# Optimization experiments

Measured on AMD Instinct MI355X. Metric: run time of the kernel, lower is better.

The kernel has to match this reference:

```python
import jax, jax.numpy as jnp
import numpy as np

N, F_IN, HID, H1, E = 50000, 512, 128, 4, 800000
NEG_SLOPE = 0.2

def setup_inputs() -> dict:
    key = jax.random.key(0)
    ks = jax.random.split(key, 10)
    s = lambda fan: 1.0 / np.sqrt(fan)
    x = jax.random.normal(ks[0], (N, F_IN), jnp.float32)
    edge_index = jax.random.randint(ks[1], (2, E), 0, N, jnp.int32)
    W1 = jax.random.normal(ks[2], (F_IN, H1 * HID), jnp.float32) * s(F_IN)
    a_src1 = jax.random.normal(ks[3], (H1, HID), jnp.float32) * s(HID)
    a_dst1 = jax.random.normal(ks[4], (H1, HID), jnp.float32) * s(HID)
    b1 = jnp.zeros((H1 * HID,), jnp.float32)
    W2 = jax.random.normal(ks[5], (H1 * HID, HID), jnp.float32) * s(H1 * HID)
    a_src2 = jax.random.normal(ks[6], (1, HID), jnp.float32) * s(HID)
    a_dst2 = jax.random.normal(ks[7], (1, HID), jnp.float32) * s(HID)
    b2 = jnp.zeros((HID,), jnp.float32)
    return {"x": x, "edge_index": edge_index, "W1": W1, "a_src1": a_src1,
            "a_dst1": a_dst1, "b1": b1, "W2": W2, "a_src2": a_src2,
            "a_dst2": a_dst2, "b2": b2}

def _gat(x, src, dst, W, a_src, a_dst, b, n):
    H, C = a_src.shape
    h = (x @ W).reshape(-1, H, C)                      # [N, H, C]
    # per-edge attention logits: alpha_src[src] + alpha_dst[dst]
    e = jax.nn.leaky_relu((h * a_src).sum(-1)[src] + (h * a_dst).sum(-1)[dst],
                          NEG_SLOPE)                   # [E', H]
    # segment softmax over destination node
    m = jax.ops.segment_max(e, dst, num_segments=n)
    p = jnp.exp(e - m[dst])
    denom = jax.ops.segment_sum(p, dst, num_segments=n)
    alpha = p / (denom[dst] + 1e-16)
    # weighted scatter-add aggregation
    out = jax.ops.segment_sum(h[src] * alpha[:, :, None], dst, num_segments=n)
    return out.reshape(-1, H * C) + b

def reference(x, edge_index, W1, a_src1, a_dst1, b1, W2, a_src2, a_dst2, b2):
    loops = jnp.arange(N, dtype=edge_index.dtype)      # add_self_loops=True
    src = jnp.concatenate([edge_index[0], loops])
    dst = jnp.concatenate([edge_index[1], loops])
    h = jax.nn.elu(_gat(x, src, dst, W1, a_src1, a_dst1, b1, N))
    return _gat(h, src, dst, W2, a_src2, a_dst2, b2, N)
```

## Files before the change

### kernel.cpp

```cpp
#include <hip/hip_runtime.h>
#include <hip/hip_bf16.h>
#include <math.h>

#define NEG_SLOPE 0.2f

constexpr int N_NODES = 50000;
constexpr int F_IN    = 512;
constexpr int HID     = 128;
constexpr int H1      = 4;
constexpr int E_EDGES = 800000;
constexpr int E_TOT   = E_EDGES + N_NODES;
constexpr int DEG_CAP = 64;

typedef __attribute__((ext_vector_type(8))) short short8;
typedef __attribute__((ext_vector_type(4))) float floatx4;
typedef __attribute__((ext_vector_type(2))) float f32x2;
typedef __attribute__((ext_vector_type(4))) unsigned short ushort4v;

__device__ __forceinline__ unsigned short f2bf(float f) {
  union { float f; unsigned int u; } v; v.f = f;
  unsigned int u = v.u + 0x7FFFu + ((v.u >> 16) & 1u);
  return (unsigned short)(u >> 16);
}
__device__ __forceinline__ float bf_lo(unsigned int u) {
  union { unsigned int u; float f; } v; v.u = u << 16; return v.f;
}
__device__ __forceinline__ float bf_hi(unsigned int u) {
  union { unsigned int u; float f; } v; v.u = u & 0xFFFF0000u; return v.f;
}

__device__ __forceinline__ void store_val(float* p, float v) { *p = v; }
__device__ __forceinline__ void store_val(unsigned short* p, float v) { *p = f2bf(v); }

template <int CPT>
__device__ __forceinline__ void store_vec(unsigned short* p, const float* v) {
#pragma unroll
  for (int c = 0; c < CPT; c += 4) {
    ushort4v o;
#pragma unroll
    for (int j = 0; j < 4; ++j) o[j] = f2bf(v[c + j]);
    *(ushort4v*)(p + c) = o;
  }
}
template <int CPT>
__device__ __forceinline__ void store_vec(float* p, const float* v) {
#pragma unroll
  for (int c = 0; c < CPT; c += 4) *(float4*)(p + c) = *(const float4*)(v + c);
}

__device__ __forceinline__ void async_load16(const void* g, void* lds) {
  __builtin_amdgcn_global_load_lds(
      (const __attribute__((address_space(1))) unsigned int*)g,
      (__attribute__((address_space(3))) unsigned int*)lds, 16, 0, 0);
}

__global__ void prep_kernel(const float* __restrict__ W1, const float* __restrict__ W2,
                            unsigned short* __restrict__ W1t, unsigned short* __restrict__ W2t,
                            int* __restrict__ cnt) {
  int i = blockIdx.x * 256 + threadIdx.x;
  if (i < N_NODES) cnt[i] = 0;
  int j = i - N_NODES;
  if (j >= 0 && j < 512 * 512) {
    int n = j >> 9, k = j & 511;
    W1t[j] = f2bf(W1[k * 512 + n]);
  }
  int l = i - N_NODES - 512 * 512;
  if (l >= 0 && l < 128 * 512) {
    int n = l >> 9, k = l & 511;
    W2t[l] = f2bf(W2[k * 128 + n]);
  }
}

template <bool CVT_A, bool FILL, typename OT>
__global__ __launch_bounds__(256) void gemm_bf16_kernel(
    const void* __restrict__ Araw, const unsigned short* __restrict__ Bt,
    OT* __restrict__ C, const float* __restrict__ a_srcp, const float* __restrict__ a_dstp,
    float* __restrict__ alpha_src, float* __restrict__ alpha_dst,
    int M, int N, int K, int Hn, int nRowTiles,
    const int* __restrict__ ei, int* __restrict__ cnt, int* __restrict__ adj,
    int gemmBlocks) {
  __shared__ unsigned short As[128 * 32];
  __shared__ unsigned short Bs[128 * 32];
  __shared__ float red_s[128][2];
  __shared__ float red_d[128][2];

  if (FILL && blockIdx.x >= gemmBlocks) {
    int i = (blockIdx.x - gemmBlocks) * 256 + threadIdx.x;
    if (i < E_TOT) {
      int s, d;
      if (i < E_EDGES) { s = ei[i]; d = ei[E_EDGES + i]; }
      else             { s = i - E_EDGES; d = s; }
      int pos = atomicAdd(&cnt[d], 1);
      if (pos < DEG_CAP) adj[d * DEG_CAP + pos] = s;
    }
    return;
  }

  int grp = blockIdx.x / (8 * Hn);
  int w8 = blockIdx.x % (8 * Hn);
  int head = w8 >> 3;
  int rowTile = grp * 8 + (w8 & 7);
  if (rowTile >= nRowTiles) return;
  int row0 = rowTile * 128;
  int col0 = head * 128;

  int tid = threadIdx.x;
  int lane = tid & 63, wave = tid >> 6;
  int wm = wave & 1, wn = wave >> 1;
  int l15 = lane & 15, quad = lane >> 4;

  floatx4 acc[4][4];
#pragma unroll
  for (int i = 0; i < 4; ++i)
#pragma unroll
    for (int j = 0; j < 4; ++j) acc[i][j] = (floatx4){0.f, 0.f, 0.f, 0.f};

  int seg_b = wave * 2;
  int r_in = (lane >> 2);
  int c8sw = (((lane & 3) ^ ((lane >> 3) & 3)) * 8);
  int sqrd = (quad ^ ((l15 >> 1) & 3)) * 8;

  for (int k0 = 0; k0 < K; k0 += 32) {
#pragma unroll
    for (int p = 0; p < 2; ++p) {
      int seg = seg_b + p;
      int r = seg * 16 + r_in;
      int gc = col0 + r;
      async_load16(Bt + (size_t)gc * K + k0 + c8sw, &Bs[seg * 512]);
    }
    if constexpr (CVT_A) {
      const float* Af = (const float*)Araw;
#pragma unroll
      for (int p = 0; p < 4; ++p) {
        int lin = tid + p * 256;
        int r = lin >> 3;
        int q = lin & 7;
        int gr = row0 + r; if (gr >= M) gr = M - 1;
        float4 f = *(const float4*)(Af + (size_t)gr * K + k0 + q * 4);
        ushort4v o;
        o[0] = f2bf(f.x); o[1] = f2bf(f.y); o[2] = f2bf(f.z); o[3] = f2bf(f.w);
        int sl = ((q >> 1) ^ ((lin >> 4) & 3));
        *(ushort4v*)&As[r * 32 + sl * 8 + (q & 1) * 4] = o;
      }
    } else {
      const unsigned short* Ab = (const unsigned short*)Araw;
#pragma unroll
      for (int p = 0; p < 2; ++p) {
        int seg = seg_b + p;
        int r = seg * 16 + r_in;
        int gr = row0 + r; if (gr >= M) gr = M - 1;
        async_load16(Ab + (size_t)gr * K + k0 + c8sw, &As[seg * 512]);
      }
    }
    __syncthreads();

    short8 a[4], b[4];
#pragma unroll
    for (int mi = 0; mi < 4; ++mi)
      a[mi] = *(const short8*)&As[(wm * 64 + mi * 16 + l15) * 32 + sqrd];
#pragma unroll
    for (int ni = 0; ni < 4; ++ni)
      b[ni] = *(const short8*)&Bs[(wn * 64 + ni * 16 + l15) * 32 + sqrd];
#pragma unroll
    for (int mi = 0; mi < 4; ++mi)
#pragma unroll
      for (int ni = 0; ni < 4; ++ni)
        acc[mi][ni] = __builtin_amdgcn_mfma_f32_16x16x32_bf16(a[mi], b[ni], acc[mi][ni], 0, 0, 0);
    __syncthreads();
  }

  float a_s[4], a_d[4];
#pragma unroll
  for (int ni = 0; ni < 4; ++ni) {
    int cih = wn * 64 + ni * 16 + l15;
    a_s[ni] = a_srcp[head * HID + cih];
    a_d[ni] = a_dstp[head * HID + cih];
  }

#pragma unroll
  for (int mi = 0; mi < 4; ++mi) {
#pragma unroll
    for (int r = 0; r < 4; ++r) {
      int rloc = wm * 64 + mi * 16 + quad * 4 + r;
      int grow = row0 + rloc;
      float ps = 0.f, pd = 0.f;
#pragma unroll
      for (int ni = 0; ni < 4; ++ni) {
        float v = acc[mi][ni][r];
        ps += v * a_s[ni];
        pd += v * a_d[ni];
        if (grow < M) {
          int gcol = col0 + wn * 64 + ni * 16 + l15;
          store_val(&C[(size_t)grow * N + gcol], v);
        }
      }
#pragma unroll
      for (int off = 1; off < 16; off <<= 1) {
        ps += __shfl_xor(ps, off);
        pd += __shfl_xor(pd, off);
      }
      if (l15 == 0) { red_s[rloc][wn] = ps; red_d[rloc][wn] = pd; }
    }
  }
  __syncthreads();
  if (tid < 128) {
    int grow = row0 + tid;
    if (grow < M) {
      alpha_src[(size_t)grow * Hn + head] = red_s[tid][0] + red_s[tid][1];
      alpha_dst[(size_t)grow * Hn + head] = red_d[tid][0] + red_d[tid][1];
    }
  }
}

template <int H, typename OT>
__global__ __launch_bounds__(64) void aggregate_kernel(
    const unsigned short* __restrict__ h, const float* __restrict__ asrc,
    const float* __restrict__ adst, const int* __restrict__ cnt,
    const int* __restrict__ adj, const float* __restrict__ bias,
    OT* __restrict__ out, int apply_elu) {
  constexpr int CPT = 8;
  constexpr int CH = H * HID;
  constexpr int NCH = CH / CPT;
  constexpr int SLOTS = 64 / NCH;
  __shared__ float p_sh[64 * H];
  __shared__ int ro_sh[64];

  const int node = blockIdx.x;
  const int lane = threadIdx.x;
  int deg = cnt[node];
  if (deg > DEG_CAP) deg = DEG_CAP;

  int s_i = 0;
  if (lane < deg) s_i = adj[node * DEG_CAP + lane];
  ro_sh[lane] = s_i * (CH * 2);
  float ar[H];
  if constexpr (H == 4) {
    float4 f = (lane < deg) ? *(const float4*)(asrc + (size_t)s_i * 4)
                            : make_float4(0.f, 0.f, 0.f, 0.f);
    ar[0] = f.x; ar[1] = f.y; ar[2] = f.z; ar[3] = f.w;
  } else {
    ar[0] = (lane < deg) ? asrc[s_i] : 0.f;
  }
  asm volatile("s_waitcnt lgkmcnt(0)" ::: "memory");

  const int chlane = lane % NCH;
  const int slot = lane / NCH;
  const int ch = chlane * CPT;
  const int head = ch >> 7;
  const char* hb = (const char*)h + ch * 2;

  auto loadu = [&](uint4& U, int e) {
    if (e < deg) U = *(const uint4*)(hb + (unsigned)ro_sh[e]);
    else         U = make_uint4(0u, 0u, 0u, 0u);
  };

  uint4 u0, u1, u2, u3, u4, u5, u6, u7;
  loadu(u0, slot);             loadu(u1, slot + SLOTS);
  loadu(u2, slot + 2 * SLOTS); loadu(u3, slot + 3 * SLOTS);
  loadu(u4, slot + 4 * SLOTS); loadu(u5, slot + 5 * SLOTS);
  loadu(u6, slot + 6 * SLOTS); loadu(u7, slot + 7 * SLOTS);

#pragma unroll
  for (int hh = 0; hh < H; ++hh) {
    float v = ar[hh] + adst[node * H + hh];
    v = (v > 0.f) ? v : NEG_SLOPE * v;
    float lg = (lane < deg) ? v : -1e30f;
#pragma unroll
    for (int o = 32; o; o >>= 1) lg = fmaxf(lg, __shfl_xor(lg, o));
    float p = (lane < deg) ? __expf(v - lg) : 0.f;
    float s = p;
#pragma unroll
    for (int o = 32; o; o >>= 1) s += __shfl_xor(s, o);
    p_sh[lane * H + hh] = p * (1.f / (s + 1e-16f));
  }
  asm volatile("s_waitcnt lgkmcnt(0)" ::: "memory");

  f32x2 ac0 = {0.f, 0.f}, ac1 = {0.f, 0.f}, ac2v = {0.f, 0.f}, ac3 = {0.f, 0.f};
  auto consume = [&](const uint4& U, int e) {
    float w = p_sh[(e & 63) * H + head];
    f32x2 wp = {w, w};
    f32x2 t;
    t.x = bf_lo(U.x); t.y = bf_hi(U.x); ac0  += t * wp;
    t.x = bf_lo(U.y); t.y = bf_hi(U.y); ac1  += t * wp;
    t.x = bf_lo(U.z); t.y = bf_hi(U.z); ac2v += t * wp;
    t.x = bf_lo(U.w); t.y = bf_hi(U.w); ac3  += t * wp;
  };

  int base = 0;
  for (;;) {
    int nb = base + 8 * SLOTS;
    if (nb < deg) {
      consume(u0, base + slot);             loadu(u0, nb + slot);
      consume(u1, base + slot + SLOTS);     loadu(u1, nb + slot + SLOTS);
      consume(u2, base + slot + 2 * SLOTS); loadu(u2, nb + slot + 2 * SLOTS);
      consume(u3, base + slot + 3 * SLOTS); loadu(u3, nb + slot + 3 * SLOTS);
      consume(u4, base + slot + 4 * SLOTS); loadu(u4, nb + slot + 4 * SLOTS);
      consume(u5, base + slot + 5 * SLOTS); loadu(u5, nb + slot + 5 * SLOTS);
      consume(u6, base + slot + 6 * SLOTS); loadu(u6, nb + slot + 6 * SLOTS);
      consume(u7, base + slot + 7 * SLOTS); loadu(u7, nb + slot + 7 * SLOTS);
      base = nb;
    } else {
      consume(u0, base + slot);             consume(u1, base + slot + SLOTS);
      consume(u2, base + slot + 2 * SLOTS); consume(u3, base + slot + 3 * SLOTS);
      consume(u4, base + slot + 4 * SLOTS); consume(u5, base + slot + 5 * SLOTS);
      consume(u6, base + slot + 6 * SLOTS); consume(u7, base + slot + 7 * SLOTS);
      break;
    }
  }

#pragma unroll
  for (int o = NCH; o < 64; o <<= 1) {
    ac0.x  += __shfl_xor(ac0.x, o);  ac0.y  += __shfl_xor(ac0.y, o);
    ac1.x  += __shfl_xor(ac1.x, o);  ac1.y  += __shfl_xor(ac1.y, o);
    ac2v.x += __shfl_xor(ac2v.x, o); ac2v.y += __shfl_xor(ac2v.y, o);
    ac3.x  += __shfl_xor(ac3.x, o);  ac3.y  += __shfl_xor(ac3.y, o);
  }

  if (slot == 0) {
    float r[CPT] = {ac0.x, ac0.y, ac1.x, ac1.y, ac2v.x, ac2v.y, ac3.x, ac3.y};
#pragma unroll
    for (int c = 0; c < CPT; ++c) {
      float t = r[c] + bias[ch + c];
      if (apply_elu) t = (t > 0.f) ? t : (__expf(t) - 1.f);
      r[c] = t;
    }
    store_vec<CPT>(&out[(size_t)node * CH + ch], r);
  }
}

extern "C" void kernel_launch(void* const* d_in, const int* in_sizes, int n_in,
                              void* d_out, int out_size, void* d_ws, size_t ws_size,
                              hipStream_t stream) {
  const float* x      = (const float*)d_in[0];
  const int*   ei     = (const int*)d_in[1];
  const float* W1     = (const float*)d_in[2];
  const float* a_src1 = (const float*)d_in[3];
  const float* a_dst1 = (const float*)d_in[4];
  const float* b1     = (const float*)d_in[5];
  const float* W2     = (const float*)d_in[6];
  const float* a_src2 = (const float*)d_in[7];
  const float* a_dst2 = (const float*)d_in[8];
  const float* b2     = (const float*)d_in[9];
  float* out = (float*)d_out;

  float* ws   = (float*)d_ws;
  float* as1  = ws;
  float* ad1  = as1 + N_NODES * H1;
  float* as2  = ad1 + N_NODES * H1;
  float* ad2  = as2 + N_NODES;
  unsigned short* bufA = (unsigned short*)(ad2 + N_NODES);
  unsigned short* bufB = bufA + (size_t)N_NODES * 512;
  unsigned short* hmidb = bufA;
  unsigned short* h1b   = bufB;
  unsigned short* h2b   = bufB;
  unsigned short* W1t   = bufB + (size_t)N_NODES * 512;
  unsigned short* W2t   = W1t + 512 * 512;
  int* cnt = (int*)(W2t + 128 * 512);
  int* adj = cnt + N_NODES;

  constexpr int NRT = (N_NODES + 127) / 128;
  constexpr int NRT8 = ((NRT + 7) / 8) * 8;
  constexpr int PREP_ITEMS = N_NODES + 512 * 512 + 128 * 512;
  constexpr int FILL_BLOCKS = (E_TOT + 255) / 256;
  constexpr int GEMM1_BLOCKS = NRT8 * H1;

  prep_kernel<<<(PREP_ITEMS + 255) / 256, 256, 0, stream>>>(W1, W2, W1t, W2t, cnt);

  gemm_bf16_kernel<true, true, unsigned short>
      <<<GEMM1_BLOCKS + FILL_BLOCKS, 256, 0, stream>>>(
      x, W1t, h1b, a_src1, a_dst1, as1, ad1, N_NODES, 512, 512, H1, NRT,
      ei, cnt, adj, GEMM1_BLOCKS);
  aggregate_kernel<4, unsigned short><<<N_NODES, 64, 0, stream>>>(
      h1b, as1, ad1, cnt, adj, b1, hmidb, 1);

  gemm_bf16_kernel<false, false, unsigned short><<<NRT8, 256, 0, stream>>>(
      hmidb, W2t, h2b, a_src2, a_dst2, as2, ad2, N_NODES, 128, 512, 1, NRT,
      nullptr, nullptr, nullptr, 0);
  aggregate_kernel<1, float><<<N_NODES, 64, 0, stream>>>(
      h2b, as2, ad2, cnt, adj, b2, out, 0);
}
```

Baseline: 466.9 us.

## Double-buffer GEMM LDS tiles and prefetch A into registers

```diff
diff --git a/kernel.cpp b/kernel.cpp
--- a/kernel.cpp
+++ b/kernel.cpp
@@ -79,8 +79,8 @@
     int M, int N, int K, int Hn, int nRowTiles,
     const int* __restrict__ ei, int* __restrict__ cnt, int* __restrict__ adj,
     int gemmBlocks) {
-  __shared__ unsigned short As[128 * 32];
-  __shared__ unsigned short Bs[128 * 32];
+  __shared__ unsigned short As[2][128 * 32];
+  __shared__ unsigned short Bs[2][128 * 32];
   __shared__ float red_s[128][2];
   __shared__ float red_d[128][2];
 
@@ -120,52 +120,91 @@
   int c8sw = (((lane & 3) ^ ((lane >> 3) & 3)) * 8);
   int sqrd = (quad ^ ((l15 >> 1) & 3)) * 8;
 
-  for (int k0 = 0; k0 < K; k0 += 32) {
+  const float* Af = (const float*)Araw;
+  const unsigned short* Ab = (const unsigned short*)Araw;
+
+  auto stageB = [&](int k0, int buf) {
 #pragma unroll
     for (int p = 0; p < 2; ++p) {
       int seg = seg_b + p;
       int r = seg * 16 + r_in;
       int gc = col0 + r;
-      async_load16(Bt + (size_t)gc * K + k0 + c8sw, &Bs[seg * 512]);
-    }
-    if constexpr (CVT_A) {
-      const float* Af = (const float*)Araw;
-#pragma unroll
-      for (int p = 0; p < 4; ++p) {
-        int lin = tid + p * 256;
-        int r = lin >> 3;
-        int q = lin & 7;
-        int gr = row0 + r; if (gr >= M) gr = M - 1;
-        float4 f = *(const float4*)(Af + (size_t)gr * K + k0 + q * 4);
-        ushort4v o;
-        o[0] = f2bf(f.x); o[1] = f2bf(f.y); o[2] = f2bf(f.z); o[3] = f2bf(f.w);
-        int sl = ((q >> 1) ^ ((lin >> 4) & 3));
-        *(ushort4v*)&As[r * 32 + sl * 8 + (q & 1) * 4] = o;
+      async_load16(Bt + (size_t)gc * K + k0 + c8sw, &Bs[buf][seg * 512]);
+    }
+  };
+  auto stageA_async = [&](int k0, int buf) {
+#pragma unroll
+    for (int p = 0; p < 2; ++p) {
+      int seg = seg_b + p;
+      int r = seg * 16 + r_in;
+      int gr = row0 + r; if (gr >= M) gr = M - 1;
+      async_load16(Ab + (size_t)gr * K + k0 + c8sw, &As[buf][seg * 512]);
+    }
+  };
+
+  float4 fA[4];
+  auto loadA_regs = [&](int k0) {
+#pragma unroll
+    for (int p = 0; p < 4; ++p) {
+      int lin = tid + p * 256;
+      int r = lin >> 3;
+      int q = lin & 7;
+      int gr = row0 + r; if (gr >= M) gr = M - 1;
+      fA[p] = *(const float4*)(Af + (size_t)gr * K + k0 + q * 4);
+    }
+  };
+  auto writeA_lds = [&](int buf) {
+#pragma unroll
+    for (int p = 0; p < 4; ++p) {
+      int lin = tid + p * 256;
+      int r = lin >> 3;
+      int q = lin & 7;
+      ushort4v o;
+      o[0] = f2bf(fA[p].x); o[1] = f2bf(fA[p].y); o[2] = f2bf(fA[p].z); o[3] = f2bf(fA[p].w);
+      int sl = ((q >> 1) ^ ((lin >> 4) & 3));
+      *(ushort4v*)&As[buf][r * 32 + sl * 8 + (q & 1) * 4] = o;
+    }
+  };
+
+  const int nsteps = K >> 5;
+
+  stageB(0, 0);
+  if constexpr (CVT_A) {
+    loadA_regs(0);
+    writeA_lds(0);
+    if (nsteps > 1) loadA_regs(32);
+  } else {
+    stageA_async(0, 0);
+  }
+  __syncthreads();
+
+  for (int t = 0; t < nsteps; ++t) {
+    int cur = t & 1, nxt = cur ^ 1;
+    int k1 = (t + 1) << 5;
+
+    if (t + 1 < nsteps) {
+      stageB(k1, nxt);
+      if constexpr (CVT_A) {
+        writeA_lds(nxt);
+        if (t + 2 < nsteps) loadA_regs(k1 + 32);
+      } else {
+        stageA_async(k1, nxt);
       }
-    } else {
-      const unsigned short* Ab = (const unsigned short*)Araw;
-#pragma unroll
-      for (int p = 0; p < 2; ++p) {
-        int seg = seg_b + p;
-        int r = seg * 16 + r_in;
-        int gr = row0 + r; if (gr >= M) gr = M - 1;
-        async_load16(Ab + (size_t)gr * K + k0 + c8sw, &As[seg * 512]);
-      }
-    }
-    __syncthreads();
+    }
 
     short8 a[4], b[4];
 #pragma unroll
     for (int mi = 0; mi < 4; ++mi)
-      a[mi] = *(const short8*)&As[(wm * 64 + mi * 16 + l15) * 32 + sqrd];
+      a[mi] = *(const short8*)&As[cur][(wm * 64 + mi * 16 + l15) * 32 + sqrd];
 #pragma unroll
     for (int ni = 0; ni < 4; ++ni)
-      b[ni] = *(const short8*)&Bs[(wn * 64 + ni * 16 + l15) * 32 + sqrd];
+      b[ni] = *(const short8*)&Bs[cur][(wn * 64 + ni * 16 + l15) * 32 + sqrd];
 #pragma unroll
     for (int mi = 0; mi < 4; ++mi)
 #pragma unroll
       for (int ni = 0; ni < 4; ++ni)
         acc[mi][ni] = __builtin_amdgcn_mfma_f32_16x16x32_bf16(a[mi], b[ni], acc[mi][ni], 0, 0, 0);
+
     __syncthreads();
   }
 
```

Result: slower. 495.5 us (+6.1%).
